# Optimization experiments

Measured on AMD Instinct MI355X. Metric: run time of the kernel, lower is better.

## Reference

```python
import jax, jax.numpy as jnp
import numpy as np

N_HEADS = 16
HEAD_DIM = 128
ROPE_BASE = 50000.0
EPS = 1e-06


def _rotate_half(x):
    half = x.shape[-1] // 2
    return jnp.concatenate([-x[..., half:], x[..., :half]], axis=-1)


def _rms_norm(x, w):
    rms = jnp.sqrt(jnp.mean(x * x, axis=-1, keepdims=True) + EPS)
    return w * (x / rms)


def _rope_tables(n, dim, dtype):
    inv_freq = 1.0 / (ROPE_BASE ** (jnp.arange(0, dim, 2, dtype=jnp.float32) / dim))
    t = jnp.arange(n, dtype=jnp.float32)
    freqs = jnp.outer(t, inv_freq)          # [n, dim/2]
    emb = jnp.concatenate([freqs, freqs], axis=-1)  # [n, dim]
    return jnp.cos(emb).astype(dtype), jnp.sin(emb).astype(dtype)


def setup_inputs() -> dict:
    key = jax.random.key(0)
    ks = jax.random.split(key, 5)
    B, n, d = 2, 2048, 2048
    inner = N_HEADS * HEAD_DIM
    s = 1.0 / np.sqrt(d)
    return {
        "x": jax.random.normal(ks[0], (B, n, d), jnp.float32),
        "Wq": jax.random.normal(ks[1], (d, inner), jnp.float32) * s,
        "Wk": jax.random.normal(ks[2], (d, inner), jnp.float32) * s,
        "Wv": jax.random.normal(ks[3], (d, inner), jnp.float32) * s,
        "Wo": jax.random.normal(ks[4], (inner, d), jnp.float32) * s,
        "qn_w": jnp.ones((inner,), jnp.float32),
        "kn_w": jnp.ones((inner,), jnp.float32),
    }


def reference(x, Wq, Wk, Wv, Wo, qn_w, kn_w):
    B, n, d = x.shape
    # QKV projections (no bias)
    q = x @ Wq
    k = x @ Wk
    v = x @ Wv
    # QK RMSNorm over full inner_dim (as in the torch module)
    q = _rms_norm(q, qn_w)
    k = _rms_norm(k, kn_w)
    # [B, H, n, Dh]
    q = q.reshape(B, n, N_HEADS, HEAD_DIM).transpose(0, 2, 1, 3)
    k = k.reshape(B, n, N_HEADS, HEAD_DIM).transpose(0, 2, 1, 3)
    v = v.reshape(B, n, N_HEADS, HEAD_DIM).transpose(0, 2, 1, 3)
    # RoPE (rotary_dim == head_dim -> full rotation)
    cos, sin = _rope_tables(n, HEAD_DIM, x.dtype)  # [n, Dh]
    cos = cos[None, None]
    sin = sin[None, None]
    q = q * cos + _rotate_half(q) * sin
    k = k * cos + _rotate_half(k) * sin
    # Causal SDPA
    scale = 1.0 / np.sqrt(HEAD_DIM)
    scores = jnp.einsum("bhqd,bhkd->bhqk", q, k) * scale
    causal = jnp.tril(jnp.ones((n, n), dtype=bool))
    scores = jnp.where(causal, scores, jnp.finfo(scores.dtype).min)
    attn = jax.nn.softmax(scores, axis=-1)
    out = jnp.einsum("bhqk,bhkd->bhqd", attn, v)
    out = out.transpose(0, 2, 1, 3).reshape(B, n, N_HEADS * HEAD_DIM)
    return out @ Wo
```

## Files before the change

kernel.cpp:

```cpp
#include <hip/hip_runtime.h>

typedef unsigned short u16;
typedef unsigned int u32;
typedef __attribute__((ext_vector_type(8))) short short8;
typedef __attribute__((ext_vector_type(4))) float f32x4;
typedef __attribute__((ext_vector_type(16))) float f32x16;
typedef __attribute__((ext_vector_type(4))) u32 u32x4;

typedef __attribute__((address_space(3))) unsigned int as3u32;
typedef __attribute__((address_space(1))) unsigned int as1u32;

__device__ __forceinline__ void gld16(void* lds, const void* g) {
    __builtin_amdgcn_global_load_lds((as1u32*)(void*)g, (as3u32*)lds, 16, 0, 0);
}

__device__ inline float bf2f(u16 u) {
    u32 v = ((u32)u) << 16;
    return __builtin_bit_cast(float, v);
}
__device__ inline u16 f2bf(float f) {
    u32 u = __builtin_bit_cast(u32, f);
    u32 r = u + 0x7FFF + ((u >> 16) & 1);
    return (u16)(r >> 16);
}
__device__ __forceinline__ u32 cvtpk_bf16(float lo, float hi) {
    u32 r;
    asm("v_cvt_pk_bf16_f32 %0, %1, %2" : "=v"(r) : "v"(lo), "v"(hi));
    return r;
}
__device__ inline void unpack8(uint4 v, float* f) {
    u32 a[4] = {v.x, v.y, v.z, v.w};
#pragma unroll
    for (int i = 0; i < 4; ++i) {
        f[2 * i]     = bf2f((u16)(a[i] & 0xffff));
        f[2 * i + 1] = bf2f((u16)(a[i] >> 16));
    }
}

__global__ __launch_bounds__(256) void cast_f32_bf16(const float* __restrict__ in,
                                                     u16* __restrict__ out, int n) {
    int i = (blockIdx.x * 256 + threadIdx.x) * 4;
    if (i >= n) return;
    float4 v = *(const float4*)&in[i];
    ushort4 o;
    o.x = f2bf(v.x); o.y = f2bf(v.y); o.z = f2bf(v.z); o.w = f2bf(v.w);
    *(ushort4*)&out[i] = o;
}

__global__ __launch_bounds__(256) void transpose_cast(const float* __restrict__ in,
                                                      u16* __restrict__ out, int dim) {
    __shared__ float tile[32][33];
    const int n0 = blockIdx.x * 32, k0 = blockIdx.y * 32;
    const int tx = threadIdx.x & 31, ty = threadIdx.x >> 5;
#pragma unroll
    for (int i = 0; i < 32; i += 8)
        tile[ty + i][tx] = in[(size_t)(k0 + ty + i) * dim + n0 + tx];
    __syncthreads();
#pragma unroll
    for (int i = 0; i < 32; i += 8)
        out[(size_t)(n0 + ty + i) * dim + k0 + tx] = f2bf(tile[tx][ty + i]);
}

__global__ __launch_bounds__(256) void rope_tables(float* __restrict__ cosb,
                                                   float* __restrict__ sinb) {
    int idx = blockIdx.x * 256 + threadIdx.x;
    int pos = idx >> 6, i = idx & 63;
    float invf = __expf(-(float)i * (10.819778284410283f / 64.0f));
    float a = (float)pos * invf;
    cosb[idx] = cosf(a);
    sinb[idx] = sinf(a);
}

template <bool BF16OUT>
__global__ __launch_bounds__(256) void gemm_bt(const u16* __restrict__ A,
                                               const u16* __restrict__ Bt,
                                               void* __restrict__ Cv,
                                               int M, int N, int K) {
    __shared__ u16 As[128][64];
    __shared__ u16 Bs[128][64];
    const int bm = blockIdx.y, bn = blockIdx.x;
    const int tid = threadIdx.x;
    const int lane = tid & 63, w = tid >> 6;
    const int wm = (w >> 1) * 64, wn = (w & 1) * 64;
    const int lrow = lane & 15;
    const int sw = (lane & 7) << 4;
    const int srl = lane >> 3;
    const int ssw = ((lane & 7) * 16) ^ (srl << 4);
    const char* AB = (const char*)A;
    const char* BB = (const char*)Bt;
    f32x4 acc[4][4] = {};

    for (int k0 = 0; k0 < K; k0 += 64) {
        __syncthreads();
#pragma unroll
        for (int i = 0; i < 4; ++i) {
            const int rb = i * 32 + w * 8;
            gld16(&As[rb][0], AB + ((size_t)(bm * 128 + rb + srl) * K + k0) * 2 + ssw);
            gld16(&Bs[rb][0], BB + ((size_t)(bn * 128 + rb + srl) * K + k0) * 2 + ssw);
        }
        __syncthreads();
        const char* AsB = (const char*)As;
        const char* BsB = (const char*)Bs;
#pragma unroll
        for (int kk = 0; kk < 2; ++kk) {
            const int cb = (kk * 64 + (lane >> 4) * 16) ^ sw;
            short8 af[4], bf_[4];
#pragma unroll
            for (int i = 0; i < 4; ++i)
                af[i] = *(const short8*)(AsB + (wm + i * 16 + lrow) * 128 + cb);
#pragma unroll
            for (int j = 0; j < 4; ++j)
                bf_[j] = *(const short8*)(BsB + (wn + j * 16 + lrow) * 128 + cb);
#pragma unroll
            for (int i = 0; i < 4; ++i)
#pragma unroll
                for (int j = 0; j < 4; ++j)
                    acc[i][j] = __builtin_amdgcn_mfma_f32_16x16x32_bf16(af[i], bf_[j], acc[i][j], 0, 0, 0);
        }
    }
    const int crow = (lane >> 4) * 4, ccol = lane & 15;
#pragma unroll
    for (int i = 0; i < 4; ++i)
#pragma unroll
        for (int j = 0; j < 4; ++j)
#pragma unroll
            for (int r = 0; r < 4; ++r) {
                size_t off = (size_t)(bm * 128 + wm + i * 16 + crow + r) * N +
                             (size_t)(bn * 128 + wn + j * 16 + ccol);
                if (BF16OUT) ((u16*)Cv)[off] = f2bf(acc[i][j][r]);
                else         ((float*)Cv)[off] = acc[i][j][r];
            }
}

__global__ __launch_bounds__(256) void norm_rope(const u16* __restrict__ qkv,
                                                 const float* __restrict__ qw,
                                                 const float* __restrict__ kw,
                                                 const float* __restrict__ cosb,
                                                 const float* __restrict__ sinb,
                                                 u16* __restrict__ Qout,
                                                 u16* __restrict__ Kout) {
    __shared__ float qf[2048];
    __shared__ float kf[2048];
    __shared__ float red[8];
    const int r = blockIdx.x;
    const int b = r >> 11, pos = r & 2047;
    const int t = threadIdx.x;
    const u16* row = qkv + (size_t)r * 6144;
    uint4 qv = *(const uint4*)&row[t * 8];
    uint4 kv = *(const uint4*)&row[2048 + t * 8];
    float qe[8], ke[8];
    unpack8(qv, qe);
    unpack8(kv, ke);
    float sq = 0.f, sk = 0.f;
#pragma unroll
    for (int e = 0; e < 8; ++e) {
        qf[t * 8 + e] = qe[e];
        kf[t * 8 + e] = ke[e];
        sq += qe[e] * qe[e];
        sk += ke[e] * ke[e];
    }
#pragma unroll
    for (int msk = 1; msk < 64; msk <<= 1) {
        sq += __shfl_xor(sq, msk);
        sk += __shfl_xor(sk, msk);
    }
    if ((t & 63) == 0) { red[t >> 6] = sq; red[4 + (t >> 6)] = sk; }
    __syncthreads();
    float ssq = red[0] + red[1] + red[2] + red[3];
    float ssk = red[4] + red[5] + red[6] + red[7];
    const float invq = 0.12751946f / sqrtf(ssq * (1.f / 2048.f) + 1e-6f);
    const float invk = 1.0f / sqrtf(ssk * (1.f / 2048.f) + 1e-6f);
    const float* ct = cosb + pos * 64;
    const float* st = sinb + pos * 64;
    u16 qo[8], ko[8];
#pragma unroll
    for (int e = 0; e < 8; ++e) {
        int c = t * 8 + e;
        int jl = c & 127;
        int hb = c & ~127;
        int jj = jl & 63;
        float cs = ct[jj], sn = st[jj];
        int pair = hb + ((jl < 64) ? jl + 64 : jl - 64);
        float sgn = (jl < 64) ? -1.f : 1.f;
        float xq = qf[c] * qw[c], pq = qf[pair] * qw[pair];
        float xk = kf[c] * kw[c], pk = kf[pair] * kw[pair];
        qo[e] = f2bf((xq * cs + sgn * pq * sn) * invq);
        ko[e] = f2bf((xk * cs + sgn * pk * sn) * invk);
    }
    const int h = (t * 8) >> 7;
    const int j0 = (t * 8) & 127;
    size_t o = ((size_t)(b * 16 + h) * 2048 + pos) * 128 + j0;
    *(uint4*)&Qout[o] = *(uint4*)qo;
    *(uint4*)&Kout[o] = *(uint4*)ko;
}

__global__ __launch_bounds__(256) void v_transpose(const u16* __restrict__ qkv,
                                                   u16* __restrict__ Vt) {
    __shared__ u16 tile[64][40];
    const int bxx = blockIdx.x;
    const int jt = bxx & 3, pt = (bxx >> 2) & 31, bh = bxx >> 7;
    const int b = bh >> 4, h = bh & 15;
    const int pos0 = pt * 64, j0 = jt * 32;
    const int t = threadIdx.x;
    {
        int p = t >> 2, jc = (t & 3) * 8;
        const u16* src = qkv + (size_t)(b * 2048 + pos0 + p) * 6144 + 4096 + h * 128 + j0 + jc;
        *(uint4*)&tile[p][jc] = *(const uint4*)src;
    }
    __syncthreads();
    {
        int j = t >> 3, pc = (t & 7) * 8;
        u16 tmp[8];
#pragma unroll
        for (int e = 0; e < 8; ++e) tmp[e] = tile[pc + e][j];
        *(uint4*)&Vt[((size_t)bh * 128 + j0 + j) * 2048 + pos0 + pc] = *(uint4*)tmp;
    }
}

__global__ __launch_bounds__(256, 1) void attn_fwd(const u16* __restrict__ Qr,
                                                   const u16* __restrict__ Kr,
                                                   const u16* __restrict__ Vt,
                                                   u16* __restrict__ O) {
    __shared__ u16 Ks[2][64][128];
    __shared__ u16 VsT[2][128][64];
    const int bx = blockIdx.x;
    const int xcd = bx & 7, sub = bx >> 3;
    const int bh = xcd + 8 * (sub & 3);
    const int pi = sub >> 2;
    const int tid = threadIdx.x;
    const int lane = tid & 63, w = tid >> 6;
    const int ql = lane & 31, h = lane >> 5;
    const char* KhB = (const char*)(Kr + (size_t)bh * 2048 * 128);
    const char* VhB = (const char*)(Vt + (size_t)bh * 128 * 2048);
    const u16* Qh = Qr + (size_t)bh * 2048 * 128;
    const int b = bh >> 4, hh = bh & 15;
    const int krl = lane >> 4;
    const int ksc = (lane & 15) * 16;
    const int vrl = lane >> 3;
    const int vsc = (lane & 7) * 16;
    const int swz = (ql & 7) << 4;

    for (int half = 0; half < 2; ++half) {
        const int qt = half ? (15 - pi) : pi;
        const int q0w = qt * 128 + w * 32;
        const int qg = q0w + ql;
        short8 qb[8];
#pragma unroll
        for (int s = 0; s < 8; ++s)
            qb[s] = *(const short8*)&Qh[(size_t)qg * 128 + s * 16 + h * 8];

        f32x16 ot[4] = {};
        float m = -3e38f, ls = 0.f;
        const int kend = qt * 128 + 128;

        __syncthreads();
#pragma unroll
        for (int j = 0; j < 4; ++j) {
            const int krb = w * 16 + j * 4;
            const int kr = krb + krl;
            gld16(&Ks[0][krb][0], KhB + (size_t)kr * 256 + (ksc ^ ((kr & 7) << 4)));
            const int vrb = w * 32 + j * 8;
            const int vr = vrb + vrl;
            gld16(&VsT[0][vrb][0], VhB + (size_t)vr * 4096 + (vsc ^ ((vr & 7) << 4)));
        }

        for (int k0 = 0; k0 < kend; k0 += 64) {
            const int buf = (k0 >> 6) & 1;
            __syncthreads();
            if (k0 + 64 < kend) {
                const int kn = k0 + 64;
#pragma unroll
                for (int j = 0; j < 4; ++j) {
                    const int krb = w * 16 + j * 4;
                    const int kr = krb + krl;
                    gld16(&Ks[buf ^ 1][krb][0],
                          KhB + (size_t)(kn + kr) * 256 + (ksc ^ ((kr & 7) << 4)));
                    const int vrb = w * 32 + j * 8;
                    const int vr = vrb + vrl;
                    gld16(&VsT[buf ^ 1][vrb][0],
                          VhB + (size_t)vr * 4096 + (size_t)kn * 2 + (vsc ^ ((vr & 7) << 4)));
                }
            }
            const char* KsB = (const char*)&Ks[buf][0][0];
            const char* VsB = (const char*)&VsT[buf][0][0];

            f32x16 st[2] = {};
#pragma unroll
            for (int s = 0; s < 8; ++s) {
                short8 kf0 = *(const short8*)(KsB + (size_t)ql * 256 + ((s * 32 + 16 * h) ^ swz));
                short8 kf1 = *(const short8*)(KsB + (size_t)(32 + ql) * 256 + ((s * 32 + 16 * h) ^ swz));
                st[0] = __builtin_amdgcn_mfma_f32_32x32x16_bf16(kf0, qb[s], st[0], 0, 0, 0);
                st[1] = __builtin_amdgcn_mfma_f32_32x32x16_bf16(kf1, qb[s], st[1], 0, 0, 0);
            }

            if (k0 + 64 > q0w) {
#pragma unroll
                for (int T = 0; T < 2; ++T)
#pragma unroll
                    for (int reg = 0; reg < 16; ++reg) {
                        int c = k0 + 32 * T + (reg & 3) + 8 * (reg >> 2) + 4 * h;
                        if (c > qg) st[T][reg] = -1e30f;
                    }
            }

            float mx = st[0][0];
#pragma unroll
            for (int T = 0; T < 2; ++T)
#pragma unroll
                for (int reg = 0; reg < 16; ++reg) mx = fmaxf(mx, st[T][reg]);
            mx = fmaxf(mx, __shfl_xor(mx, 32));

            if (__any(mx > m + 8.f)) {
                float mn = fmaxf(m, mx);
                float corr = exp2f(m - mn);
                m = mn;
                ls *= corr;
#pragma unroll
                for (int td = 0; td < 4; ++td)
#pragma unroll
                    for (int reg = 0; reg < 16; ++reg) ot[td][reg] *= corr;
            }

            float ps = 0.f;
#pragma unroll
            for (int T = 0; T < 2; ++T)
#pragma unroll
                for (int reg = 0; reg < 16; ++reg) {
                    float p = exp2f(st[T][reg] - m);
                    st[T][reg] = p;
                    ps += p;
                }
            ps += __shfl_xor(ps, 32);
            ls += ps;

#pragma unroll
            for (int T = 0; T < 2; ++T) {
                u32 c[4][2];
#pragma unroll
                for (int mm = 0; mm < 4; ++mm) {
                    c[mm][0] = cvtpk_bf16(st[T][4 * mm + 0], st[T][4 * mm + 1]);
                    c[mm][1] = cvtpk_bf16(st[T][4 * mm + 2], st[T][4 * mm + 3]);
                }
#pragma unroll
                for (int i = 0; i < 2; ++i) {
                    const int ks = 2 * T + i;
                    u32 a0 = c[2 * i][0], b0 = c[2 * i + 1][0];
                    u32 a1 = c[2 * i][1], b1 = c[2 * i + 1][1];
                    asm volatile("v_permlane32_swap_b32 %0, %1" : "+v"(a0), "+v"(b0));
                    asm volatile("v_permlane32_swap_b32 %0, %1" : "+v"(a1), "+v"(b1));
                    u32x4 pw = {a0, a1, b0, b1};
                    short8 pf = __builtin_bit_cast(short8, pw);
#pragma unroll
                    for (int td = 0; td < 4; ++td) {
                        short8 vf = *(const short8*)(VsB + (size_t)(32 * td + ql) * 128 +
                                                     ((32 * ks + 16 * h) ^ swz));
                        ot[td] = __builtin_amdgcn_mfma_f32_32x32x16_bf16(vf, pf, ot[td], 0, 0, 0);
                    }
                }
            }
        }

        const float inv = 1.0f / ls;
        const size_t base = ((size_t)b * 2048 + qg) * 2048 + (size_t)hh * 128;
#pragma unroll
        for (int td = 0; td < 4; ++td)
#pragma unroll
            for (int g = 0; g < 4; ++g) {
                ushort4 o4;
                o4.x = f2bf(ot[td][4 * g + 0] * inv);
                o4.y = f2bf(ot[td][4 * g + 1] * inv);
                o4.z = f2bf(ot[td][4 * g + 2] * inv);
                o4.w = f2bf(ot[td][4 * g + 3] * inv);
                *(ushort4*)&O[base + 32 * td + 8 * g + 4 * h] = o4;
            }
    }
}

extern "C" void kernel_launch(void* const* d_in, const int* in_sizes, int n_in,
                              void* d_out, int out_size, void* d_ws, size_t ws_size,
                              hipStream_t stream) {
    const float* x   = (const float*)d_in[0];
    const float* Wq  = (const float*)d_in[1];
    const float* Wk  = (const float*)d_in[2];
    const float* Wv  = (const float*)d_in[3];
    const float* Wo  = (const float*)d_in[4];
    const float* qnw = (const float*)d_in[5];
    const float* knw = (const float*)d_in[6];

    const size_t MB = 1ull << 20;
    char* ws = (char*)d_ws;
    u16* Xbf    = (u16*)(ws + 0);
    u16* Qr     = (u16*)(ws + 0);
    u16* Wtqkv  = (u16*)(ws + 16 * MB);
    u16* Wot    = (u16*)(ws + 40 * MB);
    u16* QKV    = (u16*)(ws + 48 * MB);
    u16* AOut   = (u16*)(ws + 48 * MB);
    float* cosb = (float*)(ws + 96 * MB);
    float* sinb = (float*)(ws + 96 * MB + 524288);
    u16* Kr     = (u16*)(ws + 97 * MB);
    u16* Vt     = (u16*)(ws + 113 * MB);

    cast_f32_bf16<<<8192, 256, 0, stream>>>(x, Xbf, 4096 * 2048);
    transpose_cast<<<dim3(64, 64), 256, 0, stream>>>(Wq, Wtqkv, 2048);
    transpose_cast<<<dim3(64, 64), 256, 0, stream>>>(Wk, Wtqkv + 2048 * 2048, 2048);
    transpose_cast<<<dim3(64, 64), 256, 0, stream>>>(Wv, Wtqkv + 2 * 2048 * 2048, 2048);
    transpose_cast<<<dim3(64, 64), 256, 0, stream>>>(Wo, Wot, 2048);
    rope_tables<<<512, 256, 0, stream>>>(cosb, sinb);

    gemm_bt<true><<<dim3(48, 32), 256, 0, stream>>>(Xbf, Wtqkv, (void*)QKV, 4096, 6144, 2048);

    norm_rope<<<4096, 256, 0, stream>>>(QKV, qnw, knw, cosb, sinb, Qr, Kr);
    v_transpose<<<4096, 256, 0, stream>>>(QKV, Vt);

    attn_fwd<<<256, 256, 0, stream>>>(Qr, Kr, Vt, AOut);

    gemm_bt<false><<<dim3(16, 32), 256, 0, stream>>>(AOut, Wot, d_out, 4096, 2048, 2048);
}
```

Measured before the change: 309.4 us.

## Split attention into one query tile per block and widen prep kernels

```diff
diff --git a/kernel.cpp b/kernel.cpp
--- a/kernel.cpp
+++ b/kernel.cpp
@@ -39,26 +39,52 @@
 
 __global__ __launch_bounds__(256) void cast_f32_bf16(const float* __restrict__ in,
                                                      u16* __restrict__ out, int n) {
-    int i = (blockIdx.x * 256 + threadIdx.x) * 4;
+    int i = (blockIdx.x * 256 + threadIdx.x) * 8;
     if (i >= n) return;
-    float4 v = *(const float4*)&in[i];
-    ushort4 o;
-    o.x = f2bf(v.x); o.y = f2bf(v.y); o.z = f2bf(v.z); o.w = f2bf(v.w);
-    *(ushort4*)&out[i] = o;
-}
-
-__global__ __launch_bounds__(256) void transpose_cast(const float* __restrict__ in,
-                                                      u16* __restrict__ out, int dim) {
-    __shared__ float tile[32][33];
-    const int n0 = blockIdx.x * 32, k0 = blockIdx.y * 32;
-    const int tx = threadIdx.x & 31, ty = threadIdx.x >> 5;
-#pragma unroll
-    for (int i = 0; i < 32; i += 8)
-        tile[ty + i][tx] = in[(size_t)(k0 + ty + i) * dim + n0 + tx];
+    float4 a = *(const float4*)&in[i];
+    float4 b = *(const float4*)&in[i + 4];
+    u16 o[8];
+    o[0] = f2bf(a.x); o[1] = f2bf(a.y); o[2] = f2bf(a.z); o[3] = f2bf(a.w);
+    o[4] = f2bf(b.x); o[5] = f2bf(b.y); o[6] = f2bf(b.z); o[7] = f2bf(b.w);
+    *(uint4*)&out[i] = *(uint4*)o;
+}
+
+__global__ __launch_bounds__(256) void transpose_cast4(const float* __restrict__ Wq,
+                                                       const float* __restrict__ Wk,
+                                                       const float* __restrict__ Wv,
+                                                       const float* __restrict__ Wo,
+                                                       u16* __restrict__ Wtqkv,
+                                                       u16* __restrict__ Wot) {
+    __shared__ float tile[64][65];
+    const float* in;
+    u16* out;
+    switch (blockIdx.z) {
+        case 0:  in = Wq; out = Wtqkv;            break;
+        case 1:  in = Wk; out = Wtqkv + 4194304;  break;
+        case 2:  in = Wv; out = Wtqkv + 8388608;  break;
+        default: in = Wo; out = Wot;              break;
+    }
+    const int n0 = blockIdx.x * 64, k0 = blockIdx.y * 64;
+    const int t = threadIdx.x;
+    const int lr = t >> 4, lc = (t & 15) * 4;
+#pragma unroll
+    for (int rep = 0; rep < 4; ++rep) {
+        float4 v = *(const float4*)&in[(size_t)(k0 + rep * 16 + lr) * 2048 + n0 + lc];
+        tile[rep * 16 + lr][lc + 0] = v.x;
+        tile[rep * 16 + lr][lc + 1] = v.y;
+        tile[rep * 16 + lr][lc + 2] = v.z;
+        tile[rep * 16 + lr][lc + 3] = v.w;
+    }
     __syncthreads();
-#pragma unroll
-    for (int i = 0; i < 32; i += 8)
-        out[(size_t)(n0 + ty + i) * dim + k0 + tx] = f2bf(tile[tx][ty + i]);
+    const int nr = t >> 3, kc = (t & 7) * 8;
+#pragma unroll
+    for (int rep = 0; rep < 2; ++rep) {
+        const int n = rep * 32 + nr;
+        u16 o[8];
+#pragma unroll
+        for (int e = 0; e < 8; ++e) o[e] = f2bf(tile[kc + e][n]);
+        *(uint4*)&out[(size_t)(n0 + n) * 2048 + k0 + kc] = *(uint4*)o;
+    }
 }
 
 __global__ __launch_bounds__(256) void rope_tables(float* __restrict__ cosb,
@@ -196,37 +222,39 @@
 
 __global__ __launch_bounds__(256) void v_transpose(const u16* __restrict__ qkv,
                                                    u16* __restrict__ Vt) {
-    __shared__ u16 tile[64][40];
-    const int bxx = blockIdx.x;
-    const int jt = bxx & 3, pt = (bxx >> 2) & 31, bh = bxx >> 7;
+    __shared__ u16 tile[64][136];
+    const int bx = blockIdx.x;
+    const int pt = bx & 31, bh = bx >> 5;
     const int b = bh >> 4, h = bh & 15;
-    const int pos0 = pt * 64, j0 = jt * 32;
+    const int pos0 = pt * 64;
     const int t = threadIdx.x;
-    {
-        int p = t >> 2, jc = (t & 3) * 8;
-        const u16* src = qkv + (size_t)(b * 2048 + pos0 + p) * 6144 + 4096 + h * 128 + j0 + jc;
-        *(uint4*)&tile[p][jc] = *(const uint4*)src;
-    }
+    const int p = t >> 4, jc = (t & 15) * 8;
+#pragma unroll
+    for (int rep = 0; rep < 4; ++rep)
+        *(uint4*)&tile[rep * 16 + p][jc] =
+            *(const uint4*)&qkv[(size_t)(b * 2048 + pos0 + rep * 16 + p) * 6144 + 4096 + h * 128 + jc];
     __syncthreads();
-    {
-        int j = t >> 3, pc = (t & 7) * 8;
+    const int j = t >> 3, pc = (t & 7) * 8;
+#pragma unroll
+    for (int rep = 0; rep < 4; ++rep) {
+        const int jj = rep * 32 + j;
         u16 tmp[8];
 #pragma unroll
-        for (int e = 0; e < 8; ++e) tmp[e] = tile[pc + e][j];
-        *(uint4*)&Vt[((size_t)bh * 128 + j0 + j) * 2048 + pos0 + pc] = *(uint4*)tmp;
-    }
-}
-
-__global__ __launch_bounds__(256, 1) void attn_fwd(const u16* __restrict__ Qr,
+        for (int e = 0; e < 8; ++e) tmp[e] = tile[pc + e][jj];
+        *(uint4*)&Vt[((size_t)bh * 128 + jj) * 2048 + pos0 + pc] = *(uint4*)tmp;
+    }
+}
+
+__global__ __launch_bounds__(256, 2) void attn_fwd(const u16* __restrict__ Qr,
                                                    const u16* __restrict__ Kr,
                                                    const u16* __restrict__ Vt,
                                                    u16* __restrict__ O) {
     __shared__ u16 Ks[2][64][128];
     __shared__ u16 VsT[2][128][64];
     const int bx = blockIdx.x;
-    const int xcd = bx & 7, sub = bx >> 3;
-    const int bh = xcd + 8 * (sub & 3);
-    const int pi = sub >> 2;
+    const int g = bx >> 3;
+    const int bh = (bx & 7) + 8 * (g & 3);
+    const int qt = (g < 32) ? (15 - (g >> 2)) : ((g >> 2) - 8);
     const int tid = threadIdx.x;
     const int lane = tid & 63, w = tid >> 6;
     const int ql = lane & 31, h = lane >> 5;
@@ -240,140 +268,136 @@
     const int vsc = (lane & 7) * 16;
     const int swz = (ql & 7) << 4;
 
-    for (int half = 0; half < 2; ++half) {
-        const int qt = half ? (15 - pi) : pi;
-        const int q0w = qt * 128 + w * 32;
-        const int qg = q0w + ql;
-        short8 qb[8];
-#pragma unroll
-        for (int s = 0; s < 8; ++s)
-            qb[s] = *(const short8*)&Qh[(size_t)qg * 128 + s * 16 + h * 8];
-
-        f32x16 ot[4] = {};
-        float m = -3e38f, ls = 0.f;
-        const int kend = qt * 128 + 128;
-
+    const int q0w = qt * 128 + w * 32;
+    const int qg = q0w + ql;
+    short8 qb[8];
+#pragma unroll
+    for (int s = 0; s < 8; ++s)
+        qb[s] = *(const short8*)&Qh[(size_t)qg * 128 + s * 16 + h * 8];
+
+    f32x16 ot[4] = {};
+    float m = -3e38f, ls = 0.f;
+    const int kend = qt * 128 + 128;
+
+#pragma unroll
+    for (int j = 0; j < 4; ++j) {
+        const int krb = w * 16 + j * 4;
+        const int kr = krb + krl;
+        gld16(&Ks[0][krb][0], KhB + (size_t)kr * 256 + (ksc ^ ((kr & 7) << 4)));
+        const int vrb = w * 32 + j * 8;
+        const int vr = vrb + vrl;
+        gld16(&VsT[0][vrb][0], VhB + (size_t)vr * 4096 + (vsc ^ ((vr & 7) << 4)));
+    }
+
+    for (int k0 = 0; k0 < kend; k0 += 64) {
+        const int buf = (k0 >> 6) & 1;
         __syncthreads();
-#pragma unroll
-        for (int j = 0; j < 4; ++j) {
-            const int krb = w * 16 + j * 4;
-            const int kr = krb + krl;
-            gld16(&Ks[0][krb][0], KhB + (size_t)kr * 256 + (ksc ^ ((kr & 7) << 4)));
-            const int vrb = w * 32 + j * 8;
-            const int vr = vrb + vrl;
-            gld16(&VsT[0][vrb][0], VhB + (size_t)vr * 4096 + (vsc ^ ((vr & 7) << 4)));
-        }
-
-        for (int k0 = 0; k0 < kend; k0 += 64) {
-            const int buf = (k0 >> 6) & 1;
-            __syncthreads();
-            if (k0 + 64 < kend) {
-                const int kn = k0 + 64;
-#pragma unroll
-                for (int j = 0; j < 4; ++j) {
-                    const int krb = w * 16 + j * 4;
-                    const int kr = krb + krl;
-                    gld16(&Ks[buf ^ 1][krb][0],
-                          KhB + (size_t)(kn + kr) * 256 + (ksc ^ ((kr & 7) << 4)));
-                    const int vrb = w * 32 + j * 8;
-                    const int vr = vrb + vrl;
-                    gld16(&VsT[buf ^ 1][vrb][0],
-                          VhB + (size_t)vr * 4096 + (size_t)kn * 2 + (vsc ^ ((vr & 7) << 4)));
+        if (k0 + 64 < kend) {
+            const int kn = k0 + 64;
+#pragma unroll
+            for (int j = 0; j < 4; ++j) {
+                const int krb = w * 16 + j * 4;
+                const int kr = krb + krl;
+                gld16(&Ks[buf ^ 1][krb][0],
+                      KhB + (size_t)(kn + kr) * 256 + (ksc ^ ((kr & 7) << 4)));
+                const int vrb = w * 32 + j * 8;
+                const int vr = vrb + vrl;
+                gld16(&VsT[buf ^ 1][vrb][0],
+                      VhB + (size_t)vr * 4096 + (size_t)kn * 2 + (vsc ^ ((vr & 7) << 4)));
+            }
+        }
+        const char* KsB = (const char*)&Ks[buf][0][0];
+        const char* VsB = (const char*)&VsT[buf][0][0];
+
+        f32x16 st[2] = {};
+#pragma unroll
+        for (int s = 0; s < 8; ++s) {
+            short8 kf0 = *(const short8*)(KsB + (size_t)ql * 256 + ((s * 32 + 16 * h) ^ swz));
+            short8 kf1 = *(const short8*)(KsB + (size_t)(32 + ql) * 256 + ((s * 32 + 16 * h) ^ swz));
+            st[0] = __builtin_amdgcn_mfma_f32_32x32x16_bf16(kf0, qb[s], st[0], 0, 0, 0);
+            st[1] = __builtin_amdgcn_mfma_f32_32x32x16_bf16(kf1, qb[s], st[1], 0, 0, 0);
+        }
+
+        if (k0 + 64 > q0w) {
+#pragma unroll
+            for (int T = 0; T < 2; ++T)
+#pragma unroll
+                for (int reg = 0; reg < 16; ++reg) {
+                    int c = k0 + 32 * T + (reg & 3) + 8 * (reg >> 2) + 4 * h;
+                    if (c > qg) st[T][reg] = -1e30f;
+                }
+        }
+
+        float mx = st[0][0];
+#pragma unroll
+        for (int T = 0; T < 2; ++T)
+#pragma unroll
+            for (int reg = 0; reg < 16; ++reg) mx = fmaxf(mx, st[T][reg]);
+        mx = fmaxf(mx, __shfl_xor(mx, 32));
+
+        if (__any(mx > m + 8.f)) {
+            float mn = fmaxf(m, mx);
+            float corr = exp2f(m - mn);
+            m = mn;
+            ls *= corr;
+#pragma unroll
+            for (int td = 0; td < 4; ++td)
+#pragma unroll
+                for (int reg = 0; reg < 16; ++reg) ot[td][reg] *= corr;
+        }
+
+        float ps = 0.f;
+#pragma unroll
+        for (int T = 0; T < 2; ++T)
+#pragma unroll
+            for (int reg = 0; reg < 16; ++reg) {
+                float p = exp2f(st[T][reg] - m);
+                st[T][reg] = p;
+                ps += p;
+            }
+        ps += __shfl_xor(ps, 32);
+        ls += ps;
+
+#pragma unroll
+        for (int T = 0; T < 2; ++T) {
+            u32 c[4][2];
+#pragma unroll
+            for (int mm = 0; mm < 4; ++mm) {
+                c[mm][0] = cvtpk_bf16(st[T][4 * mm + 0], st[T][4 * mm + 1]);
+                c[mm][1] = cvtpk_bf16(st[T][4 * mm + 2], st[T][4 * mm + 3]);
+            }
+#pragma unroll
+            for (int i = 0; i < 2; ++i) {
+                const int ks = 2 * T + i;
+                u32 a0 = c[2 * i][0], b0 = c[2 * i + 1][0];
+                u32 a1 = c[2 * i][1], b1 = c[2 * i + 1][1];
+                asm volatile("v_permlane32_swap_b32 %0, %1" : "+v"(a0), "+v"(b0));
+                asm volatile("v_permlane32_swap_b32 %0, %1" : "+v"(a1), "+v"(b1));
+                u32x4 pw = {a0, a1, b0, b1};
+                short8 pf = __builtin_bit_cast(short8, pw);
+#pragma unroll
+                for (int td = 0; td < 4; ++td) {
+                    short8 vf = *(const short8*)(VsB + (size_t)(32 * td + ql) * 128 +
+                                                 ((32 * ks + 16 * h) ^ swz));
+                    ot[td] = __builtin_amdgcn_mfma_f32_32x32x16_bf16(vf, pf, ot[td], 0, 0, 0);
                 }
             }
-            const char* KsB = (const char*)&Ks[buf][0][0];
-            const char* VsB = (const char*)&VsT[buf][0][0];
-
-            f32x16 st[2] = {};
-#pragma unroll
-            for (int s = 0; s < 8; ++s) {
-                short8 kf0 = *(const short8*)(KsB + (size_t)ql * 256 + ((s * 32 + 16 * h) ^ swz));
-                short8 kf1 = *(const short8*)(KsB + (size_t)(32 + ql) * 256 + ((s * 32 + 16 * h) ^ swz));
-                st[0] = __builtin_amdgcn_mfma_f32_32x32x16_bf16(kf0, qb[s], st[0], 0, 0, 0);
-                st[1] = __builtin_amdgcn_mfma_f32_32x32x16_bf16(kf1, qb[s], st[1], 0, 0, 0);
-            }
-
-            if (k0 + 64 > q0w) {
-#pragma unroll
-                for (int T = 0; T < 2; ++T)
-#pragma unroll
-                    for (int reg = 0; reg < 16; ++reg) {
-                        int c = k0 + 32 * T + (reg & 3) + 8 * (reg >> 2) + 4 * h;
-                        if (c > qg) st[T][reg] = -1e30f;
-                    }
-            }
-
-            float mx = st[0][0];
-#pragma unroll
-            for (int T = 0; T < 2; ++T)
-#pragma unroll
-                for (int reg = 0; reg < 16; ++reg) mx = fmaxf(mx, st[T][reg]);
-            mx = fmaxf(mx, __shfl_xor(mx, 32));
-
-            if (__any(mx > m + 8.f)) {
-                float mn = fmaxf(m, mx);
-                float corr = exp2f(m - mn);
-                m = mn;
-                ls *= corr;
-#pragma unroll
-                for (int td = 0; td < 4; ++td)
-#pragma unroll
-                    for (int reg = 0; reg < 16; ++reg) ot[td][reg] *= corr;
-            }
-
-            float ps = 0.f;
-#pragma unroll
-            for (int T = 0; T < 2; ++T)
-#pragma unroll
-                for (int reg = 0; reg < 16; ++reg) {
-                    float p = exp2f(st[T][reg] - m);
-                    st[T][reg] = p;
-                    ps += p;
-                }
-            ps += __shfl_xor(ps, 32);
-            ls += ps;
-
-#pragma unroll
-            for (int T = 0; T < 2; ++T) {
-                u32 c[4][2];
-#pragma unroll
-                for (int mm = 0; mm < 4; ++mm) {
-                    c[mm][0] = cvtpk_bf16(st[T][4 * mm + 0], st[T][4 * mm + 1]);
-                    c[mm][1] = cvtpk_bf16(st[T][4 * mm + 2], st[T][4 * mm + 3]);
-                }
-#pragma unroll
-                for (int i = 0; i < 2; ++i) {
-                    const int ks = 2 * T + i;
-                    u32 a0 = c[2 * i][0], b0 = c[2 * i + 1][0];
-                    u32 a1 = c[2 * i][1], b1 = c[2 * i + 1][1];
-                    asm volatile("v_permlane32_swap_b32 %0, %1" : "+v"(a0), "+v"(b0));
-                    asm volatile("v_permlane32_swap_b32 %0, %1" : "+v"(a1), "+v"(b1));
-                    u32x4 pw = {a0, a1, b0, b1};
-                    short8 pf = __builtin_bit_cast(short8, pw);
-#pragma unroll
-                    for (int td = 0; td < 4; ++td) {
-                        short8 vf = *(const short8*)(VsB + (size_t)(32 * td + ql) * 128 +
-                                                     ((32 * ks + 16 * h) ^ swz));
-                        ot[td] = __builtin_amdgcn_mfma_f32_32x32x16_bf16(vf, pf, ot[td], 0, 0, 0);
-                    }
-                }
-            }
-        }
-
-        const float inv = 1.0f / ls;
-        const size_t base = ((size_t)b * 2048 + qg) * 2048 + (size_t)hh * 128;
-#pragma unroll
-        for (int td = 0; td < 4; ++td)
-#pragma unroll
-            for (int g = 0; g < 4; ++g) {
-                ushort4 o4;
-                o4.x = f2bf(ot[td][4 * g + 0] * inv);
-                o4.y = f2bf(ot[td][4 * g + 1] * inv);
-                o4.z = f2bf(ot[td][4 * g + 2] * inv);
-                o4.w = f2bf(ot[td][4 * g + 3] * inv);
-                *(ushort4*)&O[base + 32 * td + 8 * g + 4 * h] = o4;
-            }
-    }
+        }
+    }
+
+    const float inv = 1.0f / ls;
+    const size_t base = ((size_t)b * 2048 + qg) * 2048 + (size_t)hh * 128;
+#pragma unroll
+    for (int td = 0; td < 4; ++td)
+#pragma unroll
+        for (int g2 = 0; g2 < 4; ++g2) {
+            ushort4 o4;
+            o4.x = f2bf(ot[td][4 * g2 + 0] * inv);
+            o4.y = f2bf(ot[td][4 * g2 + 1] * inv);
+            o4.z = f2bf(ot[td][4 * g2 + 2] * inv);
+            o4.w = f2bf(ot[td][4 * g2 + 3] * inv);
+            *(ushort4*)&O[base + 32 * td + 8 * g2 + 4 * h] = o4;
+        }
 }
 
 extern "C" void kernel_launch(void* const* d_in, const int* in_sizes, int n_in,
@@ -400,19 +424,16 @@
     u16* Kr     = (u16*)(ws + 97 * MB);
     u16* Vt     = (u16*)(ws + 113 * MB);
 
-    cast_f32_bf16<<<8192, 256, 0, stream>>>(x, Xbf, 4096 * 2048);
-    transpose_cast<<<dim3(64, 64), 256, 0, stream>>>(Wq, Wtqkv, 2048);
-    transpose_cast<<<dim3(64, 64), 256, 0, stream>>>(Wk, Wtqkv + 2048 * 2048, 2048);
-    transpose_cast<<<dim3(64, 64), 256, 0, stream>>>(Wv, Wtqkv + 2 * 2048 * 2048, 2048);
-    transpose_cast<<<dim3(64, 64), 256, 0, stream>>>(Wo, Wot, 2048);
+    cast_f32_bf16<<<4096, 256, 0, stream>>>(x, Xbf, 4096 * 2048);
+    transpose_cast4<<<dim3(32, 32, 4), 256, 0, stream>>>(Wq, Wk, Wv, Wo, Wtqkv, Wot);
     rope_tables<<<512, 256, 0, stream>>>(cosb, sinb);
 
     gemm_bt<true><<<dim3(48, 32), 256, 0, stream>>>(Xbf, Wtqkv, (void*)QKV, 4096, 6144, 2048);
 
     norm_rope<<<4096, 256, 0, stream>>>(QKV, qnw, knw, cosb, sinb, Qr, Kr);
-    v_transpose<<<4096, 256, 0, stream>>>(QKV, Vt);
-
-    attn_fwd<<<256, 256, 0, stream>>>(Qr, Kr, Vt, AOut);
+    v_transpose<<<1024, 256, 0, stream>>>(QKV, Vt);
+
+    attn_fwd<<<512, 256, 0, stream>>>(Qr, Kr, Vt, AOut);
 
     gemm_bt<false><<<dim3(16, 32), 256, 0, stream>>>(AOut, Wot, d_out, 4096, 2048, 2048);
 }
```

New measurement: 289.0 us. -6.6%, faster.
